# Kernel tuning notes

Hardware: AMD Instinct MI355X
Metric: run time of the kernel (lower is better)

## Reference

```python
import jax, jax.numpy as jnp
import numpy as np
from math import comb, factorial

N_NODES = 100000
N_EDGES = 1600000
IN_FEATS = 128
H_FEATS = 64
D = 2
POS_Q = 0.8
NEG_Q = 0.2


def calc_thetas(d):
    # theta_i[m] = coeff of x^m in (x/2)^i (1-x/2)^(d-i) / Beta(i+1, d+1-i)
    T = np.zeros((d + 1, d + 1), dtype=np.float64)
    for i in range(d + 1):
        B = factorial(i) * factorial(d - i) / factorial(d + 1)
        for j in range(d - i + 1):
            T[i, i + j] = comb(d - i, j) * ((-1.0) ** j) / (2.0 ** (i + j)) / B
    return T


def setup_inputs() -> dict:
    key = jax.random.key(0)
    ks = jax.random.split(key, 10)
    feat = jax.random.normal(ks[0], (N_NODES, IN_FEATS), dtype=jnp.float32)
    edge_pred = jax.random.normal(ks[1], (N_EDGES,), dtype=jnp.float32)
    src = jax.random.randint(ks[2], (N_EDGES,), 0, N_NODES)
    dst = jax.random.randint(ks[3], (N_EDGES,), 0, N_NODES)
    s1 = 1.0 / np.sqrt(IN_FEATS)
    s2 = 1.0 / np.sqrt(H_FEATS)
    s3 = 1.0 / np.sqrt(H_FEATS * (D + 1))
    W1 = jax.random.normal(ks[4], (IN_FEATS, H_FEATS), dtype=jnp.float32) * s1
    b1 = jnp.zeros((H_FEATS,), dtype=jnp.float32)
    W2 = jax.random.normal(ks[5], (H_FEATS, H_FEATS), dtype=jnp.float32) * s2
    b2 = jnp.zeros((H_FEATS,), dtype=jnp.float32)
    W3 = jax.random.normal(ks[6], (H_FEATS * (D + 1), H_FEATS), dtype=jnp.float32) * s3
    b3 = jnp.zeros((H_FEATS,), dtype=jnp.float32)
    return {"feat": feat, "edge_pred": edge_pred, "src": src, "dst": dst,
            "W1": W1, "b1": b1, "W2": W2, "b2": b2, "W3": W3, "b3": b3}


def _lap_powers(h, mask_f, src, dst, n, d):
    # Returns stacked [d+1, N, H]: (I - D^{-1/2} A D^{-1/2})^k h for k=0..d,
    # restricted to edges where mask_f == 1 (edge subgraph, nodes kept).
    deg = jax.ops.segment_sum(mask_f, dst, num_segments=n)            # in-degrees
    dinv = jnp.clip(deg, 1.0, None)[:, None] ** -0.5                  # [N,1]

    def step(f, _):
        hm = f * dinv
        agg = jax.ops.segment_sum(hm[src] * mask_f[:, None], dst, num_segments=n)
        f2 = f - agg * dinv
        return f2, f2

    _, Ls = jax.lax.scan(step, h, None, length=d)                     # [d,N,H]
    return jnp.concatenate([h[None], Ls], axis=0)                     # [d+1,N,H]


def reference(feat, edge_pred, src, dst, W1, b1, W2, b2, W3, b3):
    n = feat.shape[0]
    T = jnp.asarray(calc_thetas(D), dtype=feat.dtype)                 # [D+1, D+1]

    # quantile thresholds over negative / positive edge predictions
    nan = jnp.float32(jnp.nan)
    neg_thr = jnp.nanquantile(jnp.where(edge_pred <= 0, edge_pred, nan), NEG_Q)
    pos_thr = jnp.nanquantile(jnp.where(edge_pred > 0, edge_pred, nan), POS_Q)
    m_neg = (edge_pred < neg_thr).astype(feat.dtype)
    m_pos = (edge_pred > pos_thr).astype(feat.dtype)
    m_unk = ((edge_pred <= pos_thr) & (edge_pred >= neg_thr)).astype(feat.dtype)

    # per-etype MLP (dropout is identity in eval mode)
    h = jax.nn.relu(feat @ W1 + b1)
    h = jax.nn.relu(h @ W2 + b2)

    Lpos = _lap_powers(h, m_pos, src, dst, n, D)
    Lneg = _lap_powers(h, m_neg, src, dst, n, D)
    Lunk = _lap_powers(h, m_unk, src, dst, n, D)

    h_pos = jnp.einsum('k,knh->nh', T[D], Lpos)                       # convs[-1]
    h_neg = jnp.einsum('k,knh->nh', T[0], Lneg)                       # convs[0]
    h_unk = jnp.einsum('ck,knh->cnh', T[1:D], Lunk)                   # convs[1..D-1]
    h_unk = jnp.moveaxis(h_unk, 0, 1).reshape(n, -1)                  # [N,(D-1)*H]

    h_final = jnp.concatenate([h_pos, h_unk, h_neg], axis=-1)         # [N,(D+1)*H]
    out = jax.nn.relu(h_final @ W3 + b3)
    return out  # single etype -> stack+sum is identity
```

## Files before the change

kernel.cpp:

```cpp
#include <hip/hip_runtime.h>
#include <cstdint>
#include <cstddef>


#define WS_ALIGN(x) (((x) + 255) & ~(size_t)255)
#define NBLK 256
#define MAXNB 1024

typedef __attribute__((ext_vector_type(8))) short short8;
typedef __attribute__((ext_vector_type(4))) float floatx4;

struct QState {
  unsigned n_neg, n_pos;
  unsigned prefix_neg, prefix_pos;
  int rank_neg, rank_pos;
  float frac_neg, frac_pos;
  unsigned vnext_neg, vnext_pos;
  float thr_neg, thr_pos;
  int dup_neg, dup_pos;
  unsigned hist_neg[256];
  unsigned hist_pos[256];
};

__device__ __forceinline__ unsigned f2key(float v) {
  unsigned u = __float_as_uint(v);
  return (u & 0x80000000u) ? ~u : (u | 0x80000000u);
}
__device__ __forceinline__ float key2f(unsigned k) {
  unsigned u = (k & 0x80000000u) ? (k ^ 0x80000000u) : ~k;
  return __uint_as_float(u);
}

__device__ __forceinline__ unsigned short bf16rn(float x) {
  unsigned u = __float_as_uint(x);
  u = (u + 0x7FFFu + ((u >> 16) & 1u)) >> 16;
  return (unsigned short)u;
}
__device__ __forceinline__ float bf2f(unsigned short v) {
  return __uint_as_float(((unsigned)v) << 16);
}

__global__ __launch_bounds__(256) void qhist_kernel(const float* __restrict__ ep,
                                                    QState* st, int E, int round) {
  __shared__ unsigned hN[256], hP[256];
  hN[threadIdx.x] = 0u; hP[threadIdx.x] = 0u;
  __syncthreads();
  int shift = 24 - 8 * round;
  unsigned maskHi = 0u;
  if (round > 0) maskHi = 0xFFFFFFFFu << (shift + 8);
  unsigned pN = st->prefix_neg & maskHi;
  unsigned pP = st->prefix_pos & maskHi;
  int stride = gridDim.x * blockDim.x;
  for (int e = blockIdx.x * blockDim.x + threadIdx.x; e < E; e += stride) {
    float v = ep[e];
    unsigned key = f2key(v);
    if (v <= 0.f) {
      if ((key & maskHi) == pN) atomicAdd(&hN[(key >> shift) & 255], 1u);
    } else {
      if ((key & maskHi) == pP) atomicAdd(&hP[(key >> shift) & 255], 1u);
    }
  }
  __syncthreads();
  unsigned cN = hN[threadIdx.x], cP = hP[threadIdx.x];
  if (cN) atomicAdd(&st->hist_neg[threadIdx.x], cN);
  if (cP) atomicAdd(&st->hist_pos[threadIdx.x], cP);
}

__global__ __launch_bounds__(256) void qinit_kernel(QState* st) {
  __shared__ unsigned sN[256], sP[256], rN_[256], rP_[256];
  int t = threadIdx.x;
  unsigned hn = st->hist_neg[t], hp = st->hist_pos[t];
  sN[t] = hn; sP[t] = hp; rN_[t] = hn; rP_[t] = hp;
  __syncthreads();
  for (int off = 128; off > 0; off >>= 1) {
    if (t < off) { rN_[t] += rN_[t + off]; rP_[t] += rP_[t + off]; }
    __syncthreads();
  }
  if (t == 0) {
    unsigned nN = rN_[0], nP = rP_[0];
    st->n_neg = nN; st->n_pos = nP;
    float idxN = __fmul_rn(0.2f, (float)(nN - 1));
    float lowN = floorf(idxN);
    unsigned rn = (unsigned)(int)lowN;
    st->frac_neg = __fsub_rn(idxN, lowN);
    float idxP = __fmul_rn(0.8f, (float)(nP - 1));
    float lowP = floorf(idxP);
    unsigned rp = (unsigned)(int)lowP;
    st->frac_pos = __fsub_rn(idxP, lowP);
    st->vnext_neg = 0xFFFFFFFFu; st->vnext_pos = 0xFFFFFFFFu;
    {
      unsigned cum = 0, pref = 0;
      for (int b = 0; b < 256; ++b) {
        unsigned c = sN[b];
        if (rn < cum + c) { pref = ((unsigned)b) << 24; rn -= cum; break; }
        cum += c;
      }
      st->prefix_neg = pref; st->rank_neg = (int)rn;
    }
    {
      unsigned cum = 0, pref = 0;
      for (int b = 0; b < 256; ++b) {
        unsigned c = sP[b];
        if (rp < cum + c) { pref = ((unsigned)b) << 24; rp -= cum; break; }
        cum += c;
      }
      st->prefix_pos = pref; st->rank_pos = (int)rp;
    }
  }
  st->hist_neg[t] = 0u; st->hist_pos[t] = 0u;
}

__global__ void qupdate_kernel(QState* st, int round) {
  int shift = 24 - 8 * round;
  {
    unsigned cum = 0; unsigned r = (unsigned)st->rank_neg; unsigned pref = st->prefix_neg;
    for (int b = 0; b < 256; ++b) {
      unsigned c = st->hist_neg[b];
      if (r < cum + c) {
        pref |= ((unsigned)b) << shift; r -= cum;
        if (round == 3) st->dup_neg = (r + 1 < c) ? 1 : 0;
        break;
      }
      cum += c;
    }
    st->prefix_neg = pref; st->rank_neg = (int)r;
  }
  {
    unsigned cum = 0; unsigned r = (unsigned)st->rank_pos; unsigned pref = st->prefix_pos;
    for (int b = 0; b < 256; ++b) {
      unsigned c = st->hist_pos[b];
      if (r < cum + c) {
        pref |= ((unsigned)b) << shift; r -= cum;
        if (round == 3) st->dup_pos = (r + 1 < c) ? 1 : 0;
        break;
      }
      cum += c;
    }
    st->prefix_pos = pref; st->rank_pos = (int)r;
  }
  for (int i = 0; i < 256; ++i) { st->hist_neg[i] = 0u; st->hist_pos[i] = 0u; }
}

__global__ __launch_bounds__(256) void qvnext_kernel(const float* __restrict__ ep,
                                                     QState* st, int E) {
  unsigned pN = st->prefix_neg, pP = st->prefix_pos;
  unsigned mn = 0xFFFFFFFFu, mp = 0xFFFFFFFFu;
  int stride = gridDim.x * blockDim.x;
  for (int e = blockIdx.x * blockDim.x + threadIdx.x; e < E; e += stride) {
    float v = ep[e];
    unsigned key = f2key(v);
    if (v <= 0.f) { if (key > pN && key < mn) mn = key; }
    else          { if (key > pP && key < mp) mp = key; }
  }
#pragma unroll
  for (int off = 32; off > 0; off >>= 1) {
    unsigned a = (unsigned)__shfl_down((int)mn, off);
    unsigned b = (unsigned)__shfl_down((int)mp, off);
    mn = min(mn, a); mp = min(mp, b);
  }
  __shared__ unsigned wN[4], wP[4];
  int wid = threadIdx.x >> 6, lane = threadIdx.x & 63;
  if (lane == 0) { wN[wid] = mn; wP[wid] = mp; }
  __syncthreads();
  if (threadIdx.x == 0) {
    unsigned a = min(min(wN[0], wN[1]), min(wN[2], wN[3]));
    unsigned b = min(min(wP[0], wP[1]), min(wP[2], wP[3]));
    if (a != 0xFFFFFFFFu) atomicMin(&st->vnext_neg, a);
    if (b != 0xFFFFFFFFu) atomicMin(&st->vnext_pos, b);
  }
}

__global__ void qfinal_kernel(QState* st) {
  {
    float v0 = key2f(st->prefix_neg);
    float v1 = (st->dup_neg || st->vnext_neg == 0xFFFFFFFFu) ? v0 : key2f(st->vnext_neg);
    float f = st->frac_neg;
    st->thr_neg = (f > 0.f) ? __fadd_rn(v0, __fmul_rn(f, __fsub_rn(v1, v0))) : v0;
  }
  {
    float v0 = key2f(st->prefix_pos);
    float v1 = (st->dup_pos || st->vnext_pos == 0xFFFFFFFFu) ? v0 : key2f(st->vnext_pos);
    float f = st->frac_pos;
    st->thr_pos = (f > 0.f) ? __fadd_rn(v0, __fmul_rn(f, __fsub_rn(v1, v0))) : v0;
  }
}

__global__ __launch_bounds__(256) void bucket_count(const float* __restrict__ ep,
    const int* __restrict__ dst, const QState* __restrict__ st,
    int* __restrict__ rowKey, int* __restrict__ part, int N, int E, int NB) {
  __shared__ unsigned hist[MAXNB];
  for (int i = threadIdx.x; i < NB; i += 256) hist[i] = 0u;
  __syncthreads();
  float thrN = st->thr_neg, thrP = st->thr_pos;
  const int stride = NBLK * 256;
  for (int e = blockIdx.x * 256 + threadIdx.x; e < E; e += stride) {
    float v = ep[e];
    int c = (v > thrP) ? 0 : ((v < thrN) ? 2 : 1);
    int row = c * N + dst[e];
    rowKey[e] = row;
    atomicAdd(&hist[row >> 9], 1u);
  }
  __syncthreads();
  for (int i = threadIdx.x; i < NB; i += 256)
    part[blockIdx.x * NB + i] = (int)hist[i];
}

__global__ __launch_bounds__(1024) void bucket_scanA(const int* __restrict__ part,
    int* __restrict__ bucketPtr, int NB) {
  __shared__ int s[1024];
  int t = threadIdx.x;
  int tot = 0;
  if (t < NB) {
#pragma unroll 4
    for (int blk = 0; blk < NBLK; ++blk) tot += part[blk * NB + t];
  }
  s[t] = tot;
  __syncthreads();
  for (int off = 1; off < 1024; off <<= 1) {
    int x = (t >= off) ? s[t - off] : 0;
    __syncthreads();
    s[t] += x;
    __syncthreads();
  }
  int excl = s[t] - tot;
  if (t < NB) bucketPtr[t] = excl;
  if (t == NB - 1) bucketPtr[NB] = excl + tot;
}

__global__ __launch_bounds__(64) void bucket_scanB(const int* __restrict__ part,
    const int* __restrict__ bucketPtr, int* __restrict__ baseArr, int NB) {
  int b = blockIdx.x;
  if (b >= NB) return;
  int l = threadIdx.x;
  int p0 = part[(4 * l + 0) * NB + b];
  int p1 = part[(4 * l + 1) * NB + b];
  int p2 = part[(4 * l + 2) * NB + b];
  int p3 = part[(4 * l + 3) * NB + b];
  int mySum = p0 + p1 + p2 + p3;
  int v = mySum;
#pragma unroll
  for (int off = 1; off < 64; off <<= 1) {
    int x = __shfl_up(v, off);
    if (l >= off) v += x;
  }
  int base = bucketPtr[b] + (v - mySum);
  baseArr[(4 * l + 0) * NB + b] = base;
  baseArr[(4 * l + 1) * NB + b] = base + p0;
  baseArr[(4 * l + 2) * NB + b] = base + p0 + p1;
  baseArr[(4 * l + 3) * NB + b] = base + p0 + p1 + p2;
}

__global__ __launch_bounds__(256) void bucket_scatter(const int* __restrict__ rowKey,
    const int* __restrict__ src, const int* __restrict__ baseArr,
    int2* __restrict__ staged, int E, int NB) {
  __shared__ int cur[MAXNB];
  for (int i = threadIdx.x; i < NB; i += 256)
    cur[i] = baseArr[blockIdx.x * NB + i];
  __syncthreads();
  const int stride = NBLK * 256;
  for (int e = blockIdx.x * 256 + threadIdx.x; e < E; e += stride) {
    int row = rowKey[e];
    int pos = atomicAdd(&cur[row >> 9], 1);
    staged[pos] = make_int2(row, src[e]);
  }
}

__global__ __launch_bounds__(256) void bucket_build(const int2* __restrict__ staged,
    const int* __restrict__ bucketPtr, int* __restrict__ rowPtrG,
    float* __restrict__ dinv, int* __restrict__ eSrc, int nRows, int NB) {
  __shared__ int degL[512], excl2[512], cur[512], sb[256];
  int b = blockIdx.x;
  int lo = bucketPtr[b], hi = bucketPtr[b + 1];
  int rowBase = b << 9;
  int t = threadIdx.x;
  degL[t] = 0; degL[t + 256] = 0;
  __syncthreads();
  for (int e = lo + t; e < hi; e += 256)
    atomicAdd(&degL[staged[e].x - rowBase], 1);
  __syncthreads();
  int a0 = degL[2 * t], a1 = degL[2 * t + 1];
  sb[t] = a0 + a1;
  __syncthreads();
  for (int off = 1; off < 256; off <<= 1) {
    int x = (t >= off) ? sb[t - off] : 0;
    __syncthreads();
    sb[t] += x;
    __syncthreads();
  }
  int pairExcl = sb[t] - (a0 + a1);
  excl2[2 * t] = pairExcl;
  excl2[2 * t + 1] = pairExcl + a0;
  __syncthreads();
  for (int i = t; i < 512; i += 256) {
    int row = rowBase + i;
    if (row < nRows) {
      int base = lo + excl2[i];
      rowPtrG[row] = base;
      cur[i] = base;
      dinv[row] = 1.f / sqrtf(fmaxf((float)degL[i], 1.f));
    }
  }
  if (b == NB - 1 && t == 0) rowPtrG[nRows] = bucketPtr[NB];
  __syncthreads();
  for (int e = lo + t; e < hi; e += 256) {
    int2 p = staged[e];
    int pos = atomicAdd(&cur[p.x - rowBase], 1);
    eSrc[pos] = p.y;
  }
}

template<int STEP>
__global__ __launch_bounds__(256) void gather3_kernel(const unsigned short* __restrict__ f,
    const unsigned short* __restrict__ hb, unsigned short* __restrict__ outBuf,
    const int* __restrict__ rowPtr, const int* __restrict__ eSrc,
    const float* __restrict__ dinv, int N, int nRows) {
  int r = blockIdx.x * 16 + (threadIdx.x >> 4);
  if (r >= nRows) return;
  int l = threadIdx.x & 15;
  int c = r / N;
  int n = r - c * N;
  int beg = rowPtr[r], end = rowPtr[r + 1];
  const int cb = c * N;
  const int srcOfs = (STEP == 1) ? 0 : cb;
  float ax = 0.f, ay = 0.f, az = 0.f, aw = 0.f;
  float bx = 0.f, by = 0.f, bz = 0.f, bw = 0.f;
  int e = beg;
  for (; e + 4 <= end; e += 4) {
    int s0 = eSrc[e],     s1 = eSrc[e + 1];
    int s2 = eSrc[e + 2], s3 = eSrc[e + 3];
    float c0 = dinv[cb + s0], c1 = dinv[cb + s1];
    float c2 = dinv[cb + s2], c3 = dinv[cb + s3];
    ushort4 v0 = *(const ushort4*)&f[(size_t)(srcOfs + s0) * 64 + l * 4];
    ushort4 v1 = *(const ushort4*)&f[(size_t)(srcOfs + s1) * 64 + l * 4];
    ushort4 v2 = *(const ushort4*)&f[(size_t)(srcOfs + s2) * 64 + l * 4];
    ushort4 v3 = *(const ushort4*)&f[(size_t)(srcOfs + s3) * 64 + l * 4];
    ax += bf2f(v0.x) * c0; ay += bf2f(v0.y) * c0; az += bf2f(v0.z) * c0; aw += bf2f(v0.w) * c0;
    bx += bf2f(v1.x) * c1; by += bf2f(v1.y) * c1; bz += bf2f(v1.z) * c1; bw += bf2f(v1.w) * c1;
    ax += bf2f(v2.x) * c2; ay += bf2f(v2.y) * c2; az += bf2f(v2.z) * c2; aw += bf2f(v2.w) * c2;
    bx += bf2f(v3.x) * c3; by += bf2f(v3.y) * c3; bz += bf2f(v3.z) * c3; bw += bf2f(v3.w) * c3;
  }
  for (; e < end; ++e) {
    int s = eSrc[e];
    float sc = dinv[cb + s];
    ushort4 v = *(const ushort4*)&f[(size_t)(srcOfs + s) * 64 + l * 4];
    ax += bf2f(v.x) * sc; ay += bf2f(v.y) * sc;
    az += bf2f(v.z) * sc; aw += bf2f(v.w) * sc;
  }
  ax += bx; ay += by; az += bz; aw += bw;
  float di = dinv[r];
  if (STEP == 1) {
    ushort4 fv = *(const ushort4*)&f[(size_t)n * 64 + l * 4];
    ushort4 o;
    o.x = bf16rn(bf2f(fv.x) - di * ax);
    o.y = bf16rn(bf2f(fv.y) - di * ay);
    o.z = bf16rn(bf2f(fv.z) - di * az);
    o.w = bf16rn(bf2f(fv.w) - di * aw);
    *(ushort4*)&outBuf[(size_t)r * 64 + l * 4] = o;
  } else {
    const float chA[3] = {0.f, 0.f, 3.f};
    const float c1A[3] = {0.f, 3.f, -3.f};
    const float c2A[3] = {0.75f, -1.5f, 0.75f};
    float ch = chA[c], c1 = c1A[c], c2 = c2A[c];
    ushort4 fv = *(const ushort4*)&f[(size_t)r * 64 + l * 4];
    ushort4 hv = *(const ushort4*)&hb[(size_t)n * 64 + l * 4];
    float fx = bf2f(fv.x), fy = bf2f(fv.y), fz = bf2f(fv.z), fw = bf2f(fv.w);
    ushort4 o;
    o.x = bf16rn(ch * bf2f(hv.x) + c1 * fx + c2 * (fx - di * ax));
    o.y = bf16rn(ch * bf2f(hv.y) + c1 * fy + c2 * (fy - di * ay));
    o.z = bf16rn(ch * bf2f(hv.z) + c1 * fz + c2 * (fz - di * az));
    o.w = bf16rn(ch * bf2f(hv.w) + c1 * fw + c2 * (fw - di * aw));
    *(ushort4*)&outBuf[(size_t)n * 192 + c * 64 + l * 4] = o;
  }
}

template<int STEP>
__global__ __launch_bounds__(256) void gatherF_kernel(const unsigned short* __restrict__ f,
    const unsigned short* __restrict__ hb, unsigned short* __restrict__ outBuf,
    const int* __restrict__ rowPtr, const int* __restrict__ eSrc,
    const float* __restrict__ dinv, float ch, float c1, float c2, int N) {
  int n = blockIdx.x * 16 + (threadIdx.x >> 4);
  if (n >= N) return;
  int l = threadIdx.x & 15;
  int beg = rowPtr[n], end = rowPtr[n + 1];
  float ax = 0.f, ay = 0.f, az = 0.f, aw = 0.f;
  float bx = 0.f, by = 0.f, bz = 0.f, bw = 0.f;
  int e = beg;
  for (; e + 4 <= end; e += 4) {
    int s0 = eSrc[e], s1 = eSrc[e + 1], s2 = eSrc[e + 2], s3 = eSrc[e + 3];
    float c0 = dinv[s0], c1_ = dinv[s1], c2_ = dinv[s2], c3 = dinv[s3];
    ushort4 v0 = *(const ushort4*)&f[(size_t)s0 * 64 + l * 4];
    ushort4 v1 = *(const ushort4*)&f[(size_t)s1 * 64 + l * 4];
    ushort4 v2 = *(const ushort4*)&f[(size_t)s2 * 64 + l * 4];
    ushort4 v3 = *(const ushort4*)&f[(size_t)s3 * 64 + l * 4];
    ax += bf2f(v0.x) * c0; ay += bf2f(v0.y) * c0; az += bf2f(v0.z) * c0; aw += bf2f(v0.w) * c0;
    bx += bf2f(v1.x) * c1_; by += bf2f(v1.y) * c1_; bz += bf2f(v1.z) * c1_; bw += bf2f(v1.w) * c1_;
    ax += bf2f(v2.x) * c2_; ay += bf2f(v2.y) * c2_; az += bf2f(v2.z) * c2_; aw += bf2f(v2.w) * c2_;
    bx += bf2f(v3.x) * c3; by += bf2f(v3.y) * c3; bz += bf2f(v3.z) * c3; bw += bf2f(v3.w) * c3;
  }
  for (; e < end; ++e) {
    int s = eSrc[e];
    float sc = dinv[s];
    ushort4 v = *(const ushort4*)&f[(size_t)s * 64 + l * 4];
    ax += bf2f(v.x) * sc; ay += bf2f(v.y) * sc;
    az += bf2f(v.z) * sc; aw += bf2f(v.w) * sc;
  }
  ax += bx; ay += by; az += bz; aw += bw;
  float di = dinv[n];
  size_t idx = (size_t)n * 64 + l * 4;
  ushort4 fv = *(const ushort4*)&f[idx];
  float fx = bf2f(fv.x), fy = bf2f(fv.y), fz = bf2f(fv.z), fw = bf2f(fv.w);
  ushort4 o;
  if (STEP == 1) {
    o.x = bf16rn(fx - di * ax); o.y = bf16rn(fy - di * ay);
    o.z = bf16rn(fz - di * az); o.w = bf16rn(fw - di * aw);
  } else {
    ushort4 hv = *(const ushort4*)&hb[idx];
    o.x = bf16rn(ch * bf2f(hv.x) + c1 * fx + c2 * (fx - di * ax));
    o.y = bf16rn(ch * bf2f(hv.y) + c1 * fy + c2 * (fy - di * ay));
    o.z = bf16rn(ch * bf2f(hv.z) + c1 * fz + c2 * (fz - di * az));
    o.w = bf16rn(ch * bf2f(hv.w) + c1 * fw + c2 * (fw - di * aw));
  }
  *(ushort4*)&outBuf[idx] = o;
}

__global__ void wconvAll_kernel(const float* __restrict__ W1, const float* __restrict__ W2,
                                const float* __restrict__ W3,
                                unsigned short* __restrict__ Wt1,
                                unsigned short* __restrict__ Wt2,
                                unsigned short* __restrict__ Wt3) {
  int i = blockIdx.x * 256 + threadIdx.x;
  if (i < 8192) {
    int col = i >> 7, k = i & 127;
    Wt1[i] = bf16rn(W1[(size_t)k * 64 + col]);
  } else if (i < 12288) {
    int j = i - 8192;
    int col = j >> 6, k = j & 63;
    Wt2[j] = bf16rn(W2[(size_t)k * 64 + col]);
  } else if (i < 24576) {
    int j = i - 12288;
    int col = j / 192, k = j - col * 192;
    Wt3[j] = bf16rn(W3[(size_t)k * 64 + col]);
  }
}

template<int K, int ABF, int OBF>
__global__ __launch_bounds__(256) void gemm_mfma_kernel(const void* __restrict__ Ain,
    const unsigned short* __restrict__ Wt, const float* __restrict__ bias,
    void* __restrict__ Cout, int N, int accum, int finish) {
  __shared__ short As[128 * 40];
  const int tid = threadIdx.x;
  const int wave = tid >> 6, lane = tid & 63;
  const int m = lane & 15, quad = lane >> 4;
  const int rowBase = blockIdx.x * 128;
  floatx4 acc[2][4] = {};
  const int rs = tid >> 1;
  const int cs = (tid & 1) * 16;
  const int rowS = rowBase + rs;
  const int aRow0 = (wave * 32 + m) * 40 + quad * 8;
  const int aRow1 = aRow0 + 16 * 40;
  for (int kc = 0; kc < K; kc += 32) {
    short8 s0 = {0,0,0,0,0,0,0,0}, s1 = s0;
    if (rowS < N) {
      if (ABF) {
        const unsigned short* p = (const unsigned short*)Ain + (size_t)rowS * K + kc + cs;
        s0 = *(const short8*)p;
        s1 = *(const short8*)(p + 8);
      } else {
        const float* p = (const float*)Ain + (size_t)rowS * K + kc + cs;
        float4 v0 = *(const float4*)p;
        float4 v1 = *(const float4*)(p + 4);
        float4 v2 = *(const float4*)(p + 8);
        float4 v3 = *(const float4*)(p + 12);
        s0[0] = bf16rn(v0.x); s0[1] = bf16rn(v0.y); s0[2] = bf16rn(v0.z); s0[3] = bf16rn(v0.w);
        s0[4] = bf16rn(v1.x); s0[5] = bf16rn(v1.y); s0[6] = bf16rn(v1.z); s0[7] = bf16rn(v1.w);
        s1[0] = bf16rn(v2.x); s1[1] = bf16rn(v2.y); s1[2] = bf16rn(v2.z); s1[3] = bf16rn(v2.w);
        s1[4] = bf16rn(v3.x); s1[5] = bf16rn(v3.y); s1[6] = bf16rn(v3.z); s1[7] = bf16rn(v3.w);
      }
    }
    *(short8*)&As[rs * 40 + cs] = s0;
    *(short8*)&As[rs * 40 + cs + 8] = s1;
    __syncthreads();
    short8 af0 = *(const short8*)&As[aRow0];
    short8 af1 = *(const short8*)&As[aRow1];
    const unsigned short* wp = Wt + (size_t)m * K + kc + quad * 8;
#pragma unroll
    for (int ct = 0; ct < 4; ++ct) {
      short8 bf = *(const short8*)(wp + (size_t)ct * 16 * K);
      acc[0][ct] = __builtin_amdgcn_mfma_f32_16x16x32_bf16(af0, bf, acc[0][ct], 0, 0, 0);
      acc[1][ct] = __builtin_amdgcn_mfma_f32_16x16x32_bf16(af1, bf, acc[1][ct], 0, 0, 0);
    }
    __syncthreads();
  }
#pragma unroll
  for (int h = 0; h < 2; ++h) {
    const int r0 = rowBase + wave * 32 + h * 16 + quad * 4;
#pragma unroll
    for (int ct = 0; ct < 4; ++ct) {
      float b = finish ? bias[ct * 16 + m] : 0.f;
#pragma unroll
      for (int reg = 0; reg < 4; ++reg) {
        int row = r0 + reg;
        if (row < N) {
          float o = acc[h][ct][reg];
          if (OBF) {
            if (finish) o = fmaxf(o + b, 0.f);
            ((unsigned short*)Cout)[(size_t)row * 64 + ct * 16 + m] = bf16rn(o);
          } else {
            float* cp = (float*)Cout + (size_t)row * 64 + ct * 16 + m;
            if (accum) o += *cp;
            if (finish) o = fmaxf(o + b, 0.f);
            *cp = o;
          }
        }
      }
    }
  }
}

extern "C" void kernel_launch(void* const* d_in, const int* in_sizes, int n_in,
                              void* d_out, int out_size, void* d_ws, size_t ws_size,
                              hipStream_t stream) {
  const float* feat = (const float*)d_in[0];
  const float* ep   = (const float*)d_in[1];
  const int*   src  = (const int*)d_in[2];
  const int*   dst  = (const int*)d_in[3];
  const float* W1   = (const float*)d_in[4];
  const float* b1   = (const float*)d_in[5];
  const float* W2   = (const float*)d_in[6];
  const float* b2   = (const float*)d_in[7];
  const float* W3   = (const float*)d_in[8];
  const float* b3   = (const float*)d_in[9];
  float* out = (float*)d_out;
  const int N = in_sizes[0] / 128;
  const int E = in_sizes[1];
  const int nRows = 3 * N;
  const int NB = (nRows + 511) >> 9;

  char* w = (char*)d_ws;
  size_t off = 0;
  QState* st = (QState*)(w + off);           off += WS_ALIGN(sizeof(QState));
  const size_t zeroBytes = off;
  int* rowPtr = (int*)(w + off);             off += WS_ALIGN((size_t)(nRows + 1) * 4);
  float* dinv = (float*)(w + off);           off += WS_ALIGN((size_t)nRows * 4);
  int* rowKey = (int*)(w + off);             off += WS_ALIGN((size_t)E * 4);
  int* partHist = (int*)(w + off);           off += WS_ALIGN((size_t)NBLK * NB * 4);
  int* baseArr = (int*)(w + off);            off += WS_ALIGN((size_t)NBLK * NB * 4);
  int* bucketPtr = (int*)(w + off);          off += WS_ALIGN((size_t)(NB + 1) * 4);
  int2* staged = (int2*)(w + off);           off += WS_ALIGN((size_t)E * 8);
  int* eSrc = (int*)(w + off);               off += WS_ALIGN((size_t)E * 4);
  unsigned short* Wt1 = (unsigned short*)(w + off); off += WS_ALIGN((size_t)64 * 128 * 2);
  unsigned short* Wt2 = (unsigned short*)(w + off); off += WS_ALIGN((size_t)64 * 64 * 2);
  unsigned short* Wt3 = (unsigned short*)(w + off); off += WS_ALIGN((size_t)64 * 192 * 2);
  unsigned short* h_bf = (unsigned short*)(w + off); off += WS_ALIGN((size_t)N * 64 * 2);
  const size_t fusedNeed = off + (size_t)nRows * 64 * 2 + (size_t)N * 192 * 2;
  const bool fused = (ws_size >= fusedNeed);
  unsigned short* L1_bf = (unsigned short*)(w + off);
  unsigned short* combo_bf = fused
      ? (unsigned short*)(w + off + WS_ALIGN((size_t)nRows * 64 * 2))
      : (unsigned short*)(w + off + WS_ALIGN((size_t)N * 64 * 2));
  (void)n_in; (void)out_size;

  hipMemsetAsync(d_ws, 0, zeroBytes, stream);

  qhist_kernel<<<512, 256, 0, stream>>>(ep, st, E, 0);
  qinit_kernel<<<1, 256, 0, stream>>>(st);
  for (int r = 1; r < 4; ++r) {
    qhist_kernel<<<512, 256, 0, stream>>>(ep, st, E, r);
    qupdate_kernel<<<1, 1, 0, stream>>>(st, r);
  }
  qvnext_kernel<<<512, 256, 0, stream>>>(ep, st, E);
  qfinal_kernel<<<1, 1, 0, stream>>>(st);

  wconvAll_kernel<<<(24576 + 255) / 256, 256, 0, stream>>>(W1, W2, W3, Wt1, Wt2, Wt3);
  const int gb = (N + 127) / 128;
  gemm_mfma_kernel<128, 0, 1><<<gb, 256, 0, stream>>>(feat, Wt1, b1, L1_bf, N, 0, 1);
  gemm_mfma_kernel<64, 1, 1><<<gb, 256, 0, stream>>>(L1_bf, Wt2, b2, h_bf, N, 0, 1);

  bucket_count<<<NBLK, 256, 0, stream>>>(ep, dst, st, rowKey, partHist, N, E, NB);
  bucket_scanA<<<1, 1024, 0, stream>>>(partHist, bucketPtr, NB);
  bucket_scanB<<<NB, 64, 0, stream>>>(partHist, bucketPtr, baseArr, NB);
  bucket_scatter<<<NBLK, 256, 0, stream>>>(rowKey, src, baseArr, staged, E, NB);
  bucket_build<<<NB, 256, 0, stream>>>(staged, bucketPtr, rowPtr, dinv, eSrc, nRows, NB);

  if (fused) {
    const int g3 = (nRows + 15) / 16;
    gather3_kernel<1><<<g3, 256, 0, stream>>>(h_bf, h_bf, L1_bf, rowPtr, eSrc, dinv, N, nRows);
    gather3_kernel<2><<<g3, 256, 0, stream>>>(L1_bf, h_bf, combo_bf, rowPtr, eSrc, dinv, N, nRows);
    gemm_mfma_kernel<192, 1, 0><<<gb, 256, 0, stream>>>(combo_bf, Wt3, b3, out, N, 0, 1);
  } else {
    const float chArr[3] = {0.f, 0.f, 3.f};
    const float c1Arr[3] = {0.f, 3.f, -3.f};
    const float c2Arr[3] = {0.75f, -1.5f, 0.75f};
    const int ggrid = (N + 15) / 16;
    for (int c = 0; c < 3; ++c) {
      const int* rp = rowPtr + (size_t)c * N;
      const float* dv = dinv + (size_t)c * N;
      gatherF_kernel<1><<<ggrid, 256, 0, stream>>>(h_bf, nullptr, L1_bf, rp, eSrc, dv,
                                                   0.f, 0.f, 0.f, N);
      gatherF_kernel<2><<<ggrid, 256, 0, stream>>>(L1_bf, h_bf, combo_bf, rp, eSrc, dv,
                                                   chArr[c], c1Arr[c], c2Arr[c], N);
      gemm_mfma_kernel<64, 1, 0><<<gb, 256, 0, stream>>>(combo_bf, Wt2, b3, out,
                                                         N, c > 0 ? 1 : 0, c == 2 ? 1 : 0);
    }
  }
}
```

Before: 501.5 us.

## Fuse quantile radix-select steps into histogram kernel via last-block reduction

The per-round update and initial-prefix logic now runs inside the histogram kernel. The last block to finish, found through an atomic counter, does the radix-select bookkeeping and resets the shared histograms. This removes the separate single-thread init, update and final kernels. The separate next-value pass over edge_pred is also dropped: the thresholds are rewritten so that strict comparisons need only the selected key (the positive threshold) or its successor float (the negative threshold), which is exact for the masks because no data value lies between the selected key and the next one. This trades several small serial launches and one full scan for a grid-wide atomic counter and a serial tail in one block.

```diff
diff --git a/kernel.cpp b/kernel.cpp
--- a/kernel.cpp
+++ b/kernel.cpp
@@ -6,6 +6,7 @@
 #define WS_ALIGN(x) (((x) + 255) & ~(size_t)255)
 #define NBLK 256
 #define MAXNB 1024
+#define QHBLK 512
 
 typedef __attribute__((ext_vector_type(8))) short short8;
 typedef __attribute__((ext_vector_type(4))) float floatx4;
@@ -15,9 +16,9 @@
   unsigned prefix_neg, prefix_pos;
   int rank_neg, rank_pos;
   float frac_neg, frac_pos;
-  unsigned vnext_neg, vnext_pos;
   float thr_neg, thr_pos;
   int dup_neg, dup_pos;
+  unsigned barrier;
   unsigned hist_neg[256];
   unsigned hist_pos[256];
 };
@@ -43,15 +44,18 @@
 __global__ __launch_bounds__(256) void qhist_kernel(const float* __restrict__ ep,
                                                     QState* st, int E, int round) {
   __shared__ unsigned hN[256], hP[256];
-  hN[threadIdx.x] = 0u; hP[threadIdx.x] = 0u;
+  __shared__ unsigned rN_[256], rP_[256];
+  __shared__ unsigned isLast;
+  int t = threadIdx.x;
+  hN[t] = 0u; hP[t] = 0u;
   __syncthreads();
   int shift = 24 - 8 * round;
   unsigned maskHi = 0u;
   if (round > 0) maskHi = 0xFFFFFFFFu << (shift + 8);
   unsigned pN = st->prefix_neg & maskHi;
   unsigned pP = st->prefix_pos & maskHi;
-  int stride = gridDim.x * blockDim.x;
-  for (int e = blockIdx.x * blockDim.x + threadIdx.x; e < E; e += stride) {
+  int stride = QHBLK * 256;
+  for (int e = blockIdx.x * 256 + t; e < E; e += stride) {
     float v = ep[e];
     unsigned key = f2key(v);
     if (v <= 0.f) {
@@ -61,128 +65,97 @@
     }
   }
   __syncthreads();
-  unsigned cN = hN[threadIdx.x], cP = hP[threadIdx.x];
-  if (cN) atomicAdd(&st->hist_neg[threadIdx.x], cN);
-  if (cP) atomicAdd(&st->hist_pos[threadIdx.x], cP);
-}
-
-__global__ __launch_bounds__(256) void qinit_kernel(QState* st) {
-  __shared__ unsigned sN[256], sP[256], rN_[256], rP_[256];
-  int t = threadIdx.x;
-  unsigned hn = st->hist_neg[t], hp = st->hist_pos[t];
-  sN[t] = hn; sP[t] = hp; rN_[t] = hn; rP_[t] = hp;
-  __syncthreads();
-  for (int off = 128; off > 0; off >>= 1) {
-    if (t < off) { rN_[t] += rN_[t + off]; rP_[t] += rP_[t + off]; }
-    __syncthreads();
-  }
-  if (t == 0) {
-    unsigned nN = rN_[0], nP = rP_[0];
-    st->n_neg = nN; st->n_pos = nP;
-    float idxN = __fmul_rn(0.2f, (float)(nN - 1));
-    float lowN = floorf(idxN);
-    unsigned rn = (unsigned)(int)lowN;
-    st->frac_neg = __fsub_rn(idxN, lowN);
-    float idxP = __fmul_rn(0.8f, (float)(nP - 1));
-    float lowP = floorf(idxP);
-    unsigned rp = (unsigned)(int)lowP;
-    st->frac_pos = __fsub_rn(idxP, lowP);
-    st->vnext_neg = 0xFFFFFFFFu; st->vnext_pos = 0xFFFFFFFFu;
-    {
-      unsigned cum = 0, pref = 0;
-      for (int b = 0; b < 256; ++b) {
-        unsigned c = sN[b];
-        if (rn < cum + c) { pref = ((unsigned)b) << 24; rn -= cum; break; }
-        cum += c;
-      }
-      st->prefix_neg = pref; st->rank_neg = (int)rn;
-    }
-    {
-      unsigned cum = 0, pref = 0;
-      for (int b = 0; b < 256; ++b) {
-        unsigned c = sP[b];
-        if (rp < cum + c) { pref = ((unsigned)b) << 24; rp -= cum; break; }
-        cum += c;
-      }
-      st->prefix_pos = pref; st->rank_pos = (int)rp;
-    }
-  }
-  st->hist_neg[t] = 0u; st->hist_pos[t] = 0u;
-}
-
-__global__ void qupdate_kernel(QState* st, int round) {
-  int shift = 24 - 8 * round;
-  {
-    unsigned cum = 0; unsigned r = (unsigned)st->rank_neg; unsigned pref = st->prefix_neg;
-    for (int b = 0; b < 256; ++b) {
-      unsigned c = st->hist_neg[b];
-      if (r < cum + c) {
-        pref |= ((unsigned)b) << shift; r -= cum;
-        if (round == 3) st->dup_neg = (r + 1 < c) ? 1 : 0;
-        break;
-      }
-      cum += c;
-    }
-    st->prefix_neg = pref; st->rank_neg = (int)r;
-  }
-  {
-    unsigned cum = 0; unsigned r = (unsigned)st->rank_pos; unsigned pref = st->prefix_pos;
-    for (int b = 0; b < 256; ++b) {
-      unsigned c = st->hist_pos[b];
-      if (r < cum + c) {
-        pref |= ((unsigned)b) << shift; r -= cum;
-        if (round == 3) st->dup_pos = (r + 1 < c) ? 1 : 0;
-        break;
-      }
-      cum += c;
-    }
-    st->prefix_pos = pref; st->rank_pos = (int)r;
-  }
-  for (int i = 0; i < 256; ++i) { st->hist_neg[i] = 0u; st->hist_pos[i] = 0u; }
-}
-
-__global__ __launch_bounds__(256) void qvnext_kernel(const float* __restrict__ ep,
-                                                     QState* st, int E) {
-  unsigned pN = st->prefix_neg, pP = st->prefix_pos;
-  unsigned mn = 0xFFFFFFFFu, mp = 0xFFFFFFFFu;
-  int stride = gridDim.x * blockDim.x;
-  for (int e = blockIdx.x * blockDim.x + threadIdx.x; e < E; e += stride) {
-    float v = ep[e];
-    unsigned key = f2key(v);
-    if (v <= 0.f) { if (key > pN && key < mn) mn = key; }
-    else          { if (key > pP && key < mp) mp = key; }
-  }
-#pragma unroll
-  for (int off = 32; off > 0; off >>= 1) {
-    unsigned a = (unsigned)__shfl_down((int)mn, off);
-    unsigned b = (unsigned)__shfl_down((int)mp, off);
-    mn = min(mn, a); mp = min(mp, b);
-  }
-  __shared__ unsigned wN[4], wP[4];
-  int wid = threadIdx.x >> 6, lane = threadIdx.x & 63;
-  if (lane == 0) { wN[wid] = mn; wP[wid] = mp; }
-  __syncthreads();
-  if (threadIdx.x == 0) {
-    unsigned a = min(min(wN[0], wN[1]), min(wN[2], wN[3]));
-    unsigned b = min(min(wP[0], wP[1]), min(wP[2], wP[3]));
-    if (a != 0xFFFFFFFFu) atomicMin(&st->vnext_neg, a);
-    if (b != 0xFFFFFFFFu) atomicMin(&st->vnext_pos, b);
-  }
-}
-
-__global__ void qfinal_kernel(QState* st) {
-  {
-    float v0 = key2f(st->prefix_neg);
-    float v1 = (st->dup_neg || st->vnext_neg == 0xFFFFFFFFu) ? v0 : key2f(st->vnext_neg);
-    float f = st->frac_neg;
-    st->thr_neg = (f > 0.f) ? __fadd_rn(v0, __fmul_rn(f, __fsub_rn(v1, v0))) : v0;
-  }
-  {
-    float v0 = key2f(st->prefix_pos);
-    float v1 = (st->dup_pos || st->vnext_pos == 0xFFFFFFFFu) ? v0 : key2f(st->vnext_pos);
-    float f = st->frac_pos;
-    st->thr_pos = (f > 0.f) ? __fadd_rn(v0, __fmul_rn(f, __fsub_rn(v1, v0))) : v0;
-  }
+  unsigned cN = hN[t], cP = hP[t];
+  if (cN) atomicAdd(&st->hist_neg[t], cN);
+  if (cP) atomicAdd(&st->hist_pos[t], cP);
+  __threadfence();
+  if (t == 0) isLast = (atomicAdd(&st->barrier, 1u) == (unsigned)(QHBLK - 1)) ? 1u : 0u;
+  __syncthreads();
+  if (!isLast) return;
+  __threadfence();
+  unsigned hn = atomicAdd(&st->hist_neg[t], 0u);
+  unsigned hp = atomicAdd(&st->hist_pos[t], 0u);
+  hN[t] = hn; hP[t] = hp;
+  if (round == 0) {
+    rN_[t] = hn; rP_[t] = hp;
+    __syncthreads();
+    for (int off = 128; off > 0; off >>= 1) {
+      if (t < off) { rN_[t] += rN_[t + off]; rP_[t] += rP_[t + off]; }
+      __syncthreads();
+    }
+    if (t == 0) {
+      unsigned nN = rN_[0], nP = rP_[0];
+      st->n_neg = nN; st->n_pos = nP;
+      float idxN = __fmul_rn(0.2f, (float)(nN - 1));
+      float lowN = floorf(idxN);
+      unsigned rn = (unsigned)(int)lowN;
+      st->frac_neg = __fsub_rn(idxN, lowN);
+      float idxP = __fmul_rn(0.8f, (float)(nP - 1));
+      float lowP = floorf(idxP);
+      unsigned rp = (unsigned)(int)lowP;
+      st->frac_pos = __fsub_rn(idxP, lowP);
+      {
+        unsigned cum = 0, pref = 0;
+        for (int b = 0; b < 256; ++b) {
+          unsigned c = hN[b];
+          if (rn < cum + c) { pref = ((unsigned)b) << 24; rn -= cum; break; }
+          cum += c;
+        }
+        st->prefix_neg = pref; st->rank_neg = (int)rn;
+      }
+      {
+        unsigned cum = 0, pref = 0;
+        for (int b = 0; b < 256; ++b) {
+          unsigned c = hP[b];
+          if (rp < cum + c) { pref = ((unsigned)b) << 24; rp -= cum; break; }
+          cum += c;
+        }
+        st->prefix_pos = pref; st->rank_pos = (int)rp;
+      }
+    }
+  } else {
+    __syncthreads();
+    if (t == 0) {
+      int dupN = 0, dupP = 0;
+      unsigned prefN, prefP;
+      {
+        unsigned cum = 0; unsigned r = (unsigned)st->rank_neg; unsigned pref = st->prefix_neg;
+        for (int b = 0; b < 256; ++b) {
+          unsigned c = hN[b];
+          if (r < cum + c) {
+            pref |= ((unsigned)b) << shift; r -= cum;
+            if (round == 3) dupN = (r + 1 < c) ? 1 : 0;
+            break;
+          }
+          cum += c;
+        }
+        st->prefix_neg = pref; st->rank_neg = (int)r; prefN = pref;
+      }
+      {
+        unsigned cum = 0; unsigned r = (unsigned)st->rank_pos; unsigned pref = st->prefix_pos;
+        for (int b = 0; b < 256; ++b) {
+          unsigned c = hP[b];
+          if (r < cum + c) {
+            pref |= ((unsigned)b) << shift; r -= cum;
+            if (round == 3) dupP = (r + 1 < c) ? 1 : 0;
+            break;
+          }
+          cum += c;
+        }
+        st->prefix_pos = pref; st->rank_pos = (int)r; prefP = pref;
+      }
+      if (round == 3) {
+        st->dup_neg = dupN; st->dup_pos = dupP;
+        st->thr_pos = key2f(prefP);
+        st->thr_neg = (st->frac_neg > 0.f && !dupN) ? key2f(prefN + 1u)
+                                                    : key2f(prefN);
+      }
+    }
+  }
+  __syncthreads();
+  st->hist_neg[t] = 0u;
+  st->hist_pos[t] = 0u;
+  if (t == 0) st->barrier = 0u;
 }
 
 __global__ __launch_bounds__(256) void bucket_count(const float* __restrict__ ep,
@@ -562,14 +535,8 @@
 
   hipMemsetAsync(d_ws, 0, zeroBytes, stream);
 
-  qhist_kernel<<<512, 256, 0, stream>>>(ep, st, E, 0);
-  qinit_kernel<<<1, 256, 0, stream>>>(st);
-  for (int r = 1; r < 4; ++r) {
-    qhist_kernel<<<512, 256, 0, stream>>>(ep, st, E, r);
-    qupdate_kernel<<<1, 1, 0, stream>>>(st, r);
-  }
-  qvnext_kernel<<<512, 256, 0, stream>>>(ep, st, E);
-  qfinal_kernel<<<1, 1, 0, stream>>>(st);
+  for (int r = 0; r < 4; ++r)
+    qhist_kernel<<<QHBLK, 256, 0, stream>>>(ep, st, E, r);
 
   wconvAll_kernel<<<(24576 + 255) / 256, 256, 0, stream>>>(W1, W2, W3, Wt1, Wt2, Wt3);
   const int gb = (N + 127) / 128;
```

New measurement: 554.1 us. 1.1x slower.
